# Kernel tuning notes

Measured on AMD Instinct MI355X. Metric: run time of the kernel, lower is better.

The kernel has to match this reference:

```python
import jax, jax.numpy as jnp
import numpy as np

N_NODES = 50000


def setup_inputs() -> dict:
    key = jax.random.key(0)
    k1, k2, k3, k4 = jax.random.split(key, 4)
    x = jax.random.normal(k1, (N_NODES, 128), dtype=jnp.float32)
    edge_index = jax.random.randint(k2, (2, 1600000), 0, N_NODES, dtype=jnp.int64)
    W1 = jax.random.normal(k3, (128, 256), dtype=jnp.float32) * (1.0 / np.sqrt(128))
    b1 = jnp.zeros((256,), dtype=jnp.float32)
    W2 = jax.random.normal(k4, (256, 1), dtype=jnp.float32) * (1.0 / np.sqrt(256))
    b2 = jnp.zeros((1,), dtype=jnp.float32)
    return {"x": x, "edge_index": edge_index, "W1": W1, "b1": b1, "W2": W2, "b2": b2}


def _gcn_conv(x, src, dst, norm, W, b, n_nodes):
    # PyG GCNConv: h = X W; out_i = sum_j norm_ij * h_j (+ self loop) + b
    h = x @ W                               # [N, F_out]
    msg = h[src] * norm[:, None]            # [E', F_out] gather + scale
    out = jax.ops.segment_sum(msg, dst, num_segments=n_nodes)  # scatter-add
    return out + b


def reference(x, edge_index, W1, b1, W2, b2):
    n = x.shape[0]
    loop = jnp.arange(n, dtype=edge_index.dtype)
    src = jnp.concatenate([edge_index[0], loop])   # add self loops
    dst = jnp.concatenate([edge_index[1], loop])
    # symmetric degree normalization on A + I
    deg = jax.ops.segment_sum(jnp.ones_like(dst, dtype=x.dtype), dst, num_segments=n)
    dis = jnp.where(deg > 0, jax.lax.rsqrt(deg), 0.0)
    norm = dis[src] * dis[dst]                     # [E']
    h = jax.nn.relu(_gcn_conv(x, src, dst, norm, W1, b1, n))
    return _gcn_conv(h, src, dst, norm, W2, b2, n)
```

## Files before the change

kernel.cpp:

```cpp
#include <hip/hip_runtime.h>


#define EPB_LOG 12
#define EPB (1 << EPB_LOG)
#define BW_LOG 7
#define BW (1 << BW_LOG)
#define MAXBUCK 512
#define SCAN_TILE 2048
#define AMSTRIDE 136

typedef __attribute__((ext_vector_type(8))) short bf16x8;
typedef __attribute__((ext_vector_type(4))) float f32x4;

__device__ inline unsigned short f2bf(float f) {
    unsigned int b = __float_as_uint(f);
    unsigned int r = b + 0x7FFFu + ((b >> 16) & 1u);
    return (unsigned short)(r >> 16);
}
__device__ inline float bf_lo(unsigned int u) { return __uint_as_float(u << 16); }
__device__ inline float bf_hi(unsigned int u) { return __uint_as_float(u & 0xFFFF0000u); }

__device__ inline void acc8(float* a, uint4 v) {
    a[0] += bf_lo(v.x); a[1] += bf_hi(v.x);
    a[2] += bf_lo(v.y); a[3] += bf_hi(v.y);
    a[4] += bf_lo(v.z); a[5] += bf_hi(v.z);
    a[6] += bf_lo(v.w); a[7] += bf_hi(v.w);
}

__device__ inline int detect_stride(const int* edges, int t, int* sh) {
    if (t < 64) {
        int v = edges[2 * t + 1];
        unsigned long long bb = __ballot(v != 0);
        if (t == 0) *sh = bb ? 1 : 2;
    }
    __syncthreads();
    return *sh;
}


__global__ __launch_bounds__(256) void k_count(
        const int* __restrict__ edges, const float* __restrict__ W1,
        unsigned short* __restrict__ w1t, int* __restrict__ btot_raw,
        long long E, int nbuck, int nsb) {
    int b = blockIdx.x, t = threadIdx.x;
    if (b >= nsb) {
        int row = (b - nsb) * 2 + (t >> 7);
        int k = t & 127;
        w1t[row * 128 + k] = f2bf(W1[k * 256 + row]);
        return;
    }
    __shared__ int bins[MAXBUCK];
    __shared__ int sh;
    for (int i = t; i < nbuck; i += 256) bins[i] = 0;
    int stride = detect_stride(edges, t, &sh);
    long long base = (long long)b << EPB_LOG;
    long long rem = E - base;
    int nE = (rem < (long long)EPB) ? (int)rem : EPB;
    for (int i = t; i < nE; i += 256) {
        int d = edges[(E + base + i) * stride];
        atomicAdd(&bins[d >> BW_LOG], 1);
    }
    __syncthreads();
    for (int i = t; i < nbuck; i += 256)
        if (bins[i]) atomicAdd(&btot_raw[i], bins[i]);
}

__global__ __launch_bounds__(256) void k_btot_scan(
        const int* __restrict__ btot_raw, int* __restrict__ btot,
        int* __restrict__ curg, int nbuck) {
    __shared__ int ws4[4];
    int t = threadIdx.x;
    int c4 = (nbuck + 255) >> 8;
    int lo = t * c4;
    int hi = lo + c4; if (hi > nbuck) hi = nbuck;
    if (lo > nbuck) lo = nbuck;
    int vals[2];
    int local = 0;
    for (int i = lo; i < hi; ++i) { vals[i - lo] = btot_raw[i]; local += vals[i - lo]; }
    int lane = t & 63, w = t >> 6;
    int inc = local;
    for (int off = 1; off < 64; off <<= 1) {
        int u = __shfl_up(inc, off, 64);
        if (lane >= off) inc += u;
    }
    if (lane == 63) ws4[w] = inc;
    __syncthreads();
    int woff = 0;
    for (int i = 0; i < w; ++i) woff += ws4[i];
    int ex = woff + inc - local;
    for (int i = lo; i < hi; ++i) {
        btot[i] = ex; curg[i] = ex;
        ex += vals[i - lo];
    }
}

__global__ __launch_bounds__(256) void k_partition(
        const int* __restrict__ edges, int* __restrict__ curg,
        unsigned int* __restrict__ part, long long E, int nbuck) {
    __shared__ unsigned int stage[EPB];
    __shared__ unsigned short dst16[EPB];
    __shared__ int bins[MAXBUCK];
    __shared__ int lcur[MAXBUCK];
    __shared__ int gbase[MAXBUCK];
    __shared__ int ws4[4];
    __shared__ int sh;
    int sb = blockIdx.x, t = threadIdx.x;
    for (int i = t; i < nbuck; i += 256) bins[i] = 0;
    int stride = detect_stride(edges, t, &sh);
    long long base = (long long)sb << EPB_LOG;
    long long rem = E - base;
    int nE = (rem < (long long)EPB) ? (int)rem : EPB;
    for (int i = t; i < nE; i += 256) {
        int d = edges[(E + base + i) * stride];
        dst16[i] = (unsigned short)d;
        atomicAdd(&bins[d >> BW_LOG], 1);
    }
    __syncthreads();
    int c4 = (nbuck + 255) >> 8;
    int lo = t * c4;
    int hi = lo + c4; if (hi > nbuck) hi = nbuck;
    if (lo > nbuck) lo = nbuck;
    int vals[2];
    int local = 0;
    for (int i = lo; i < hi; ++i) { vals[i - lo] = bins[i]; local += vals[i - lo]; }
    for (int i = t; i < nbuck; i += 256) {
        int c = bins[i];
        gbase[i] = c ? atomicAdd(&curg[i], c) : 0;
    }
    __syncthreads();
    int lane = t & 63, w = t >> 6;
    int inc = local;
    for (int off = 1; off < 64; off <<= 1) {
        int u = __shfl_up(inc, off, 64);
        if (lane >= off) inc += u;
    }
    if (lane == 63) ws4[w] = inc;
    __syncthreads();
    int woff = 0;
    for (int i = 0; i < w; ++i) woff += ws4[i];
    int ex = woff + inc - local;
    for (int i = lo; i < hi; ++i) {
        bins[i] = ex;
        lcur[i] = ex;
        ex += vals[i - lo];
    }
    __syncthreads();
    for (int i = t; i < nE; i += 256) {
        int s = edges[(base + i) * stride];
        int d = dst16[i];
        int b = d >> BW_LOG;
        int p = atomicAdd(&lcur[b], 1);
        stage[p] = ((unsigned int)s << 16) | (unsigned int)d;
    }
    __syncthreads();
    for (int i = t; i < nE; i += 256) {
        unsigned int pk = stage[i];
        int b = (int)(pk & 0xFFFFu) >> BW_LOG;
        part[gbase[b] + (i - bins[b])] = pk;
    }
}

__global__ __launch_bounds__(256) void k_build_csr(
        const unsigned int* __restrict__ part, const int* __restrict__ btot,
        const float* __restrict__ x, int* __restrict__ row_start,
        float* __restrict__ dis, int* __restrict__ csr_src,
        unsigned short* __restrict__ xs, int nbuck, int n, long long E) {
    __shared__ int c128[BW];
    __shared__ int lcur[BW];
    __shared__ float dld[BW];
    __shared__ int ws2[2];
    int b = blockIdx.x, t = threadIdx.x;
    if (t < BW) c128[t] = 0;
    __syncthreads();
    int start = btot[b];
    int endp = (b + 1 < nbuck) ? btot[b + 1] : (int)E;
    for (int i = start + t; i < endp; i += 256)
        atomicAdd(&c128[part[i] & (BW - 1)], 1);
    __syncthreads();
    int lane = t & 63, w = t >> 6;
    int deg = (t < BW) ? c128[t] : 0;
    int inc = deg;
    for (int off = 1; off < 64; off <<= 1) {
        int u = __shfl_up(inc, off, 64);
        if (lane >= off) inc += u;
    }
    if (t < BW && lane == 63) ws2[w] = inc;
    __syncthreads();
    if (t < BW) {
        int ex = inc - deg + ((w == 1) ? ws2[0] : 0);
        lcur[t] = ex;
        int d = (b << BW_LOG) + t;
        if (d < n) {
            row_start[d] = start + ex;
            float dv = rsqrtf((float)deg + 1.0f);
            dis[d] = dv;
            dld[t] = dv;
        }
    }
    if (b == nbuck - 1 && t == 0) row_start[n] = (int)E;
    __syncthreads();
    for (int i = start + t; i < endp; i += 256) {
        unsigned int pk = part[i];
        int r = atomicAdd(&lcur[pk & (BW - 1)], 1);
        csr_src[start + r] = (int)(pk >> 16);
    }
    int d0 = b << BW_LOG;
    for (int idx = t; idx < BW * 32; idx += 256) {
        int node = d0 + (idx >> 5);
        if (node >= n) break;
        float dv = dld[idx >> 5];
        float4 v = ((const float4*)x)[(size_t)node * 32 + (idx & 31)];
        ushort4 o;
        o.x = f2bf(v.x * dv); o.y = f2bf(v.y * dv);
        o.z = f2bf(v.z * dv); o.w = f2bf(v.w * dv);
        ((ushort4*)xs)[(size_t)node * 32 + (idx & 31)] = o;
    }
}

__global__ __launch_bounds__(256) void k_agg_mm(
        const unsigned short* __restrict__ xs, const int* __restrict__ csr_src,
        const int* __restrict__ rs, const float* __restrict__ dis,
        const unsigned short* __restrict__ w1t, const float* __restrict__ b1,
        const float* __restrict__ W2, float* __restrict__ svs, int n) {
    __shared__ short am[16 * AMSTRIDE];
    int t = threadIdx.x;
    int lane = t & 63, w = t >> 6;
    int q = lane >> 4, l16 = lane & 15;
    int blk = blockIdx.x;
    int r = w * 4 + q;
    int node = blk * 16 + r;
    const uint4* xs4 = (const uint4*)xs;

    uint4 o = {0u, 0u, 0u, 0u};
    if (node < n) {
        float a[8] = {0.f, 0.f, 0.f, 0.f, 0.f, 0.f, 0.f, 0.f};
        acc8(a, xs4[((size_t)node << 4) + l16]);
        int start = rs[node], end = rs[node + 1];
        int e = start;
        for (; e + 8 <= end; e += 8) {
            int s0 = csr_src[e],     s1 = csr_src[e + 1];
            int s2 = csr_src[e + 2], s3 = csr_src[e + 3];
            int s4 = csr_src[e + 4], s5 = csr_src[e + 5];
            int s6 = csr_src[e + 6], s7 = csr_src[e + 7];
            uint4 v0 = xs4[((size_t)s0 << 4) + l16];
            uint4 v1 = xs4[((size_t)s1 << 4) + l16];
            uint4 v2 = xs4[((size_t)s2 << 4) + l16];
            uint4 v3 = xs4[((size_t)s3 << 4) + l16];
            uint4 v4 = xs4[((size_t)s4 << 4) + l16];
            uint4 v5 = xs4[((size_t)s5 << 4) + l16];
            uint4 v6 = xs4[((size_t)s6 << 4) + l16];
            uint4 v7 = xs4[((size_t)s7 << 4) + l16];
            acc8(a, v0); acc8(a, v1); acc8(a, v2); acc8(a, v3);
            acc8(a, v4); acc8(a, v5); acc8(a, v6); acc8(a, v7);
        }
        for (; e < end; ++e) {
            int s0 = csr_src[e];
            acc8(a, xs4[((size_t)s0 << 4) + l16]);
        }
        float dn = dis[node];
        o.x = (unsigned int)f2bf(a[0] * dn) | ((unsigned int)f2bf(a[1] * dn) << 16);
        o.y = (unsigned int)f2bf(a[2] * dn) | ((unsigned int)f2bf(a[3] * dn) << 16);
        o.z = (unsigned int)f2bf(a[4] * dn) | ((unsigned int)f2bf(a[5] * dn) << 16);
        o.w = (unsigned int)f2bf(a[6] * dn) | ((unsigned int)f2bf(a[7] * dn) << 16);
    }
    *(uint4*)&am[r * AMSTRIDE + l16 * 8] = o;
    __syncthreads();
    if (w) return;
    int m = lane & 15;
    int quad = lane >> 4;
    int node0 = blk * 16;

    bf16x8 afrag[4];
    const short* arow = &am[m * AMSTRIDE + quad * 8];
#pragma unroll
    for (int ks = 0; ks < 4; ++ks)
        afrag[ks] = *(const bf16x8*)(arow + ks * 32);

    float p0 = 0.f, p1 = 0.f, p2 = 0.f, p3 = 0.f;
#pragma unroll 1
    for (int tt = 0; tt < 16; ++tt) {
        const unsigned short* brow = w1t + (size_t)(tt * 16 + m) * 128 + quad * 8;
        f32x4 acc = {0.f, 0.f, 0.f, 0.f};
#pragma unroll
        for (int ks = 0; ks < 4; ++ks) {
            bf16x8 bfrag = *(const bf16x8*)(brow + ks * 32);
            acc = __builtin_amdgcn_mfma_f32_16x16x32_bf16(afrag[ks], bfrag, acc, 0, 0, 0);
        }
        int col = tt * 16 + m;
        float bb = b1[col], w2 = W2[col];
        float h0 = acc[0] + bb, h1 = acc[1] + bb, h2 = acc[2] + bb, h3 = acc[3] + bb;
        p0 += (h0 > 0.f ? h0 : 0.f) * w2;
        p1 += (h1 > 0.f ? h1 : 0.f) * w2;
        p2 += (h2 > 0.f ? h2 : 0.f) * w2;
        p3 += (h3 > 0.f ? h3 : 0.f) * w2;
    }
#pragma unroll
    for (int off = 1; off < 16; off <<= 1) {
        p0 += __shfl_xor(p0, off, 64);
        p1 += __shfl_xor(p1, off, 64);
        p2 += __shfl_xor(p2, off, 64);
        p3 += __shfl_xor(p3, off, 64);
    }
    if (m == 0) {
        int nb = node0 + quad * 4;
        if (nb + 0 < n) svs[nb + 0] = p0 * dis[nb + 0];
        if (nb + 1 < n) svs[nb + 1] = p1 * dis[nb + 1];
        if (nb + 2 < n) svs[nb + 2] = p2 * dis[nb + 2];
        if (nb + 3 < n) svs[nb + 3] = p3 * dis[nb + 3];
    }
}

__global__ __launch_bounds__(256) void k_out(
        const float* __restrict__ svs, const int* __restrict__ csr_src,
        const int* __restrict__ row_start, const float* __restrict__ dis,
        const float* __restrict__ b2, float* __restrict__ out, int n) {
    int t = threadIdx.x;
    int lane = t & 63, w = t >> 6;
    int q = lane >> 4, l16 = lane & 15;
    int node = blockIdx.x * 16 + w * 4 + q;
    if (node >= n) return;
    int start = row_start[node], end = row_start[node + 1];
    float acc = 0.f;
    for (int e = start + l16; e < end; e += 16)
        acc += svs[csr_src[e]];
#pragma unroll
    for (int off = 1; off < 16; off <<= 1) acc += __shfl_xor(acc, off, 64);
    if (l16 == 0)
        out[node] = dis[node] * (acc + svs[node]) + b2[0];
}

__global__ void k_init(const int* __restrict__ edges, int* __restrict__ flag,
                       int* __restrict__ cnt, int n) {
    int i = blockIdx.x * blockDim.x + threadIdx.x;
    if (i < n) cnt[i] = 0;
    if (blockIdx.x == 0 && threadIdx.x < 64) {
        int v = edges[2 * threadIdx.x + 1];
        unsigned long long b = __ballot(v != 0);
        if (threadIdx.x == 0) flag[0] = b ? 1 : 2;
    }
}
__global__ __launch_bounds__(128) void k_prep_w(const float* __restrict__ W1,
        unsigned short* __restrict__ w1t) {
    int nn = blockIdx.x, k = threadIdx.x;
    w1t[nn * 128 + k] = f2bf(W1[k * 256 + nn]);
}
__global__ __launch_bounds__(256) void k_prep_xs(const float* __restrict__ x,
        const float* __restrict__ dis, unsigned short* __restrict__ xs, int n) {
    int i = blockIdx.x * 256 + threadIdx.x;
    if (i >= n * 32) return;
    float dsc = dis[i >> 5];
    float4 v = ((const float4*)x)[i];
    ushort4 o;
    o.x = f2bf(v.x * dsc); o.y = f2bf(v.y * dsc);
    o.z = f2bf(v.z * dsc); o.w = f2bf(v.w * dsc);
    ((ushort4*)xs)[i] = o;
}
__global__ void k_count_slow(const int* __restrict__ edges, const int* __restrict__ flag,
                             int* __restrict__ cnt, int* __restrict__ posi, long long E) {
    long long e = (long long)blockIdx.x * blockDim.x + threadIdx.x;
    if (e >= E) return;
    int stride = flag[0];
    int d = edges[(E + e) * stride];
    posi[e] = atomicAdd(&cnt[d], 1);
}
__global__ __launch_bounds__(256) void k_scan_partial(
        const int* __restrict__ cnt, int* __restrict__ bsum, int n) {
    int t = threadIdx.x;
    int idx = blockIdx.x * SCAN_TILE + t * 8;
    int s = 0;
#pragma unroll
    for (int j = 0; j < 8; ++j) { int i = idx + j; if (i < n) s += cnt[i]; }
    for (int off = 32; off; off >>= 1) s += __shfl_down(s, off, 64);
    __shared__ int ws[4];
    if ((t & 63) == 0) ws[t >> 6] = s;
    __syncthreads();
    if (t == 0) bsum[blockIdx.x] = ws[0] + ws[1] + ws[2] + ws[3];
}
__global__ void k_scan_tops(int* __restrict__ bsum, int nb) {
    int t = threadIdx.x;
    int w = (t < nb) ? bsum[t] : 0;
    int v = w;
    for (int off = 1; off < 64; off <<= 1) {
        int u = __shfl_up(v, off, 64);
        if (t >= off) v += u;
    }
    if (t < nb) bsum[t] = v - w;
}
__global__ __launch_bounds__(256) void k_scan_apply(
        const int* __restrict__ cnt, const int* __restrict__ bsum,
        int* __restrict__ row_start, float* __restrict__ dis, int n) {
    int t = threadIdx.x;
    int lane = t & 63, w = t >> 6;
    int idx = blockIdx.x * SCAN_TILE + t * 8;
    int vals[8];
    int s = 0;
#pragma unroll
    for (int j = 0; j < 8; ++j) { int i = idx + j; vals[j] = (i < n) ? cnt[i] : 0; s += vals[j]; }
    int inc = s;
    for (int off = 1; off < 64; off <<= 1) {
        int u = __shfl_up(inc, off, 64);
        if (lane >= off) inc += u;
    }
    __shared__ int wsum[4];
    if (lane == 63) wsum[w] = inc;
    __syncthreads();
    int woff = 0;
    for (int i = 0; i < w; ++i) woff += wsum[i];
    int ex = bsum[blockIdx.x] + woff + inc - s;
#pragma unroll
    for (int j = 0; j < 8; ++j) {
        int i = idx + j;
        if (i < n) {
            row_start[i] = ex;
            dis[i] = rsqrtf((float)vals[j] + 1.0f);
            ex += vals[j];
        }
    }
    if (idx <= n && n < idx + 8) row_start[n] = ex;
}
__global__ void k_scatter_slow(const int* __restrict__ edges, const int* __restrict__ flag,
                               const int* __restrict__ row_start, const int* __restrict__ posi,
                               int* __restrict__ csr_src, long long E) {
    long long e = (long long)blockIdx.x * blockDim.x + threadIdx.x;
    if (e >= E) return;
    int stride = flag[0];
    int s = edges[e * stride];
    int d = edges[(E + e) * stride];
    csr_src[row_start[d] + posi[e]] = s;
}
__global__ __launch_bounds__(256) void k_agg(
        const unsigned short* __restrict__ xs, const int* __restrict__ csr_src,
        const int* __restrict__ row_start, const float* __restrict__ dis,
        unsigned short* __restrict__ aggh, int n) {
    int wid  = (blockIdx.x * blockDim.x + threadIdx.x) >> 6;
    int lane = threadIdx.x & 63;
    if (wid >= n) return;
    int start = row_start[wid], end = row_start[wid + 1];
    unsigned int self = ((const unsigned int*)xs)[((size_t)wid << 6) + lane];
    float a0 = bf_lo(self), a1 = bf_hi(self);
    for (int e = start; e < end; ++e) {
        int s0 = csr_src[e];
        unsigned int v0 = ((const unsigned int*)xs)[((size_t)s0 << 6) + lane];
        a0 += bf_lo(v0); a1 += bf_hi(v0);
    }
    float dn = dis[wid];
    unsigned int pack = (unsigned int)f2bf(a0 * dn) | ((unsigned int)f2bf(a1 * dn) << 16);
    ((unsigned int*)aggh)[((size_t)wid << 6) + lane] = pack;
}
__global__ __launch_bounds__(256) void k_mm(
        const unsigned short* __restrict__ aggh, const unsigned short* __restrict__ w1t,
        const float* __restrict__ b1, const float* __restrict__ W2,
        const float* __restrict__ dis, float* __restrict__ svs, int n) {
    int wave = threadIdx.x >> 6;
    int lane = threadIdx.x & 63;
    int m = lane & 15, quad = lane >> 4;
    int node0 = blockIdx.x * 64 + wave * 16;
    bf16x8 afrag[4];
    const unsigned short* arow = aggh + (size_t)(node0 + m) * 128 + quad * 8;
#pragma unroll
    for (int ks = 0; ks < 4; ++ks) afrag[ks] = *(const bf16x8*)(arow + ks * 32);
    float p0 = 0.f, p1 = 0.f, p2 = 0.f, p3 = 0.f;
#pragma unroll 1
    for (int tt = 0; tt < 16; ++tt) {
        const unsigned short* brow = w1t + (size_t)(tt * 16 + m) * 128 + quad * 8;
        f32x4 acc = {0.f, 0.f, 0.f, 0.f};
#pragma unroll
        for (int ks = 0; ks < 4; ++ks) {
            bf16x8 bfrag = *(const bf16x8*)(brow + ks * 32);
            acc = __builtin_amdgcn_mfma_f32_16x16x32_bf16(afrag[ks], bfrag, acc, 0, 0, 0);
        }
        int col = tt * 16 + m;
        float bb = b1[col], w2 = W2[col];
        float h0 = acc[0] + bb, h1 = acc[1] + bb, h2 = acc[2] + bb, h3 = acc[3] + bb;
        p0 += (h0 > 0.f ? h0 : 0.f) * w2;
        p1 += (h1 > 0.f ? h1 : 0.f) * w2;
        p2 += (h2 > 0.f ? h2 : 0.f) * w2;
        p3 += (h3 > 0.f ? h3 : 0.f) * w2;
    }
#pragma unroll
    for (int off = 1; off < 16; off <<= 1) {
        p0 += __shfl_xor(p0, off, 64);
        p1 += __shfl_xor(p1, off, 64);
        p2 += __shfl_xor(p2, off, 64);
        p3 += __shfl_xor(p3, off, 64);
    }
    if (m == 0) {
        int nb = node0 + quad * 4;
        if (nb + 0 < n) svs[nb + 0] = p0 * dis[nb + 0];
        if (nb + 1 < n) svs[nb + 1] = p1 * dis[nb + 1];
        if (nb + 2 < n) svs[nb + 2] = p2 * dis[nb + 2];
        if (nb + 3 < n) svs[nb + 3] = p3 * dis[nb + 3];
    }
}

extern "C" void kernel_launch(void* const* d_in, const int* in_sizes, int n_in,
                              void* d_out, int out_size, void* d_ws, size_t ws_size,
                              hipStream_t stream) {
    const float* x  = (const float*)d_in[0];
    const int*   ei = (const int*)d_in[1];
    const float* W1 = (const float*)d_in[2];
    const float* b1 = (const float*)d_in[3];
    const float* W2 = (const float*)d_in[4];
    const float* b2 = (const float*)d_in[5];
    float* out = (float*)d_out;

    const int N = in_sizes[0] / 128;
    const long long E = in_sizes[1] / 2;
    const int nsb = (int)((E + EPB - 1) >> EPB_LOG);
    const int nbuck = (N + BW - 1) >> BW_LOG;

    char* ws = (char*)d_ws;
    size_t off = 0;
    auto take = [&](size_t bytes) -> char* {
        char* p = ws + off;
        off = (off + bytes + 255) & ~(size_t)255;
        return p;
    };
    int*            flag     = (int*)take(4);
    int*            cnt      = (int*)take((size_t)N * 4);
    int*            rs       = (int*)take((size_t)(N + 1) * 4);
    float*          dis      = (float*)take((size_t)N * 4);
    float*          svs      = (float*)take((size_t)N * 4);
    int*            bsum     = (int*)take(64 * 4);
    int*            btot_raw = (int*)take(MAXBUCK * 4);
    int*            btot     = (int*)take(MAXBUCK * 4);
    int*            curg     = (int*)take(MAXBUCK * 4);
    unsigned int*   part     = (unsigned int*)take((size_t)E * 4);
    int*            csr_src  = (int*)take((size_t)E * 4);
    unsigned short* xs       = (unsigned short*)take((size_t)N * 128 * 2);
    unsigned short* w1t      = (unsigned short*)take((size_t)256 * 128 * 2);
    unsigned short* aggh     = (unsigned short*)take((size_t)(N + 64) * 128 * 2);

    int nb_n  = (N + 255) / 256;
    int nb_e  = (int)((E + 255) / 256);
    int nb_s  = (N + SCAN_TILE - 1) / SCAN_TILE;
    int nb_x  = (N * 32 + 255) / 256;
    int nb_am = (N + 15) / 16;
    int nb_o  = (N + 15) / 16;

    bool fast = (N < 65536);

    if (fast) {
        hipMemsetAsync(btot_raw, 0, (size_t)nbuck * 4, stream);
        k_count    <<<nsb + 128, 256, 0, stream>>>(ei, W1, w1t, btot_raw, E, nbuck, nsb);
        k_btot_scan<<<1, 256, 0, stream>>>(btot_raw, btot, curg, nbuck);
        k_partition<<<nsb, 256, 0, stream>>>(ei, curg, part, E, nbuck);
        k_build_csr<<<nbuck, 256, 0, stream>>>(part, btot, x, rs, dis, csr_src,
                                               xs, nbuck, N, E);
        k_agg_mm   <<<nb_am, 256, 0, stream>>>(xs, csr_src, rs, dis, w1t, b1, W2, svs, N);
        k_out      <<<nb_o, 256, 0, stream>>>(svs, csr_src, rs, dis, b2, out, N);
    } else {
        k_init        <<<nb_n, 256, 0, stream>>>(ei, flag, cnt, N);
        k_prep_w      <<<256, 128, 0, stream>>>(W1, w1t);
        k_count_slow  <<<nb_e, 256, 0, stream>>>(ei, flag, cnt, (int*)part, E);
        k_scan_partial<<<nb_s, 256, 0, stream>>>(cnt, bsum, N);
        k_scan_tops   <<<1, 64, 0, stream>>>(bsum, nb_s);
        k_scan_apply  <<<nb_s, 256, 0, stream>>>(cnt, bsum, rs, dis, N);
        k_prep_xs     <<<nb_x, 256, 0, stream>>>(x, dis, xs, N);
        k_scatter_slow<<<nb_e, 256, 0, stream>>>(ei, flag, rs, (const int*)part, csr_src, E);
        k_agg         <<<(N + 3) / 4, 256, 0, stream>>>(xs, csr_src, rs, dis, aggh, N);
        k_mm          <<<(N + 63) / 64, 256, 0, stream>>>(aggh, w1t, b1, W2, dis, svs, N);
        k_out         <<<nb_o, 256, 0, stream>>>(svs, csr_src, rs, dis, b2, out, N);
    }
}
```

Before: 219.1 us.

## Enlarge agg_mm blocks to 64 nodes and prefetch neighbor indices via shuffles

The fused aggregate+matmul kernel now runs 1024-thread blocks covering 64 nodes, so four wavefronts run the MFMA stage instead of one while the other twelve exit. In the gather loop each 16-lane group loads 16 edge indices cooperatively, prefetches the next 16, and broadcasts them with shuffles, so sixteen row gathers are in flight per step. The aim is to cut serialized index loads and raise memory-level parallelism. In exchange, the larger blocks and the launch-bounds hint of 1024 threads with 8 waves per EU may raise register pressure or limit occupancy.

```diff
diff --git a/kernel.cpp b/kernel.cpp
--- a/kernel.cpp
+++ b/kernel.cpp
@@ -217,18 +217,19 @@
     }
 }
 
-__global__ __launch_bounds__(256) void k_agg_mm(
+__global__ __launch_bounds__(1024, 8) void k_agg_mm(
         const unsigned short* __restrict__ xs, const int* __restrict__ csr_src,
         const int* __restrict__ rs, const float* __restrict__ dis,
         const unsigned short* __restrict__ w1t, const float* __restrict__ b1,
         const float* __restrict__ W2, float* __restrict__ svs, int n) {
-    __shared__ short am[16 * AMSTRIDE];
+    __shared__ short am[64 * AMSTRIDE];
     int t = threadIdx.x;
     int lane = t & 63, w = t >> 6;
     int q = lane >> 4, l16 = lane & 15;
+    int qb = lane & 48;
     int blk = blockIdx.x;
     int r = w * 4 + q;
-    int node = blk * 16 + r;
+    int node = blk * 64 + r;
     const uint4* xs4 = (const uint4*)xs;
 
     uint4 o = {0u, 0u, 0u, 0u};
@@ -237,21 +238,28 @@
         acc8(a, xs4[((size_t)node << 4) + l16]);
         int start = rs[node], end = rs[node + 1];
         int e = start;
-        for (; e + 8 <= end; e += 8) {
-            int s0 = csr_src[e],     s1 = csr_src[e + 1];
-            int s2 = csr_src[e + 2], s3 = csr_src[e + 3];
-            int s4 = csr_src[e + 4], s5 = csr_src[e + 5];
-            int s6 = csr_src[e + 6], s7 = csr_src[e + 7];
-            uint4 v0 = xs4[((size_t)s0 << 4) + l16];
-            uint4 v1 = xs4[((size_t)s1 << 4) + l16];
-            uint4 v2 = xs4[((size_t)s2 << 4) + l16];
-            uint4 v3 = xs4[((size_t)s3 << 4) + l16];
-            uint4 v4 = xs4[((size_t)s4 << 4) + l16];
-            uint4 v5 = xs4[((size_t)s5 << 4) + l16];
-            uint4 v6 = xs4[((size_t)s6 << 4) + l16];
-            uint4 v7 = xs4[((size_t)s7 << 4) + l16];
-            acc8(a, v0); acc8(a, v1); acc8(a, v2); acc8(a, v3);
-            acc8(a, v4); acc8(a, v5); acc8(a, v6); acc8(a, v7);
+        int idx = 0;
+        if (e + 16 <= end) idx = csr_src[e + l16];
+        for (; e + 16 <= end; e += 16) {
+            int pe = e + 16 + l16;
+            int nidx = csr_src[pe < end ? pe : start];
+            int sA[8];
+#pragma unroll
+            for (int j = 0; j < 8; ++j) sA[j] = __shfl(idx, qb + j, 64);
+            uint4 va[8];
+#pragma unroll
+            for (int j = 0; j < 8; ++j) va[j] = xs4[((size_t)sA[j] << 4) + l16];
+#pragma unroll
+            for (int j = 0; j < 8; ++j) acc8(a, va[j]);
+            int sB[8];
+#pragma unroll
+            for (int j = 0; j < 8; ++j) sB[j] = __shfl(idx, qb + 8 + j, 64);
+            uint4 vb[8];
+#pragma unroll
+            for (int j = 0; j < 8; ++j) vb[j] = xs4[((size_t)sB[j] << 4) + l16];
+#pragma unroll
+            for (int j = 0; j < 8; ++j) acc8(a, vb[j]);
+            idx = nidx;
         }
         for (; e < end; ++e) {
             int s0 = csr_src[e];
@@ -265,13 +273,13 @@
     }
     *(uint4*)&am[r * AMSTRIDE + l16 * 8] = o;
     __syncthreads();
-    if (w) return;
+    if (w >= 4) return;
     int m = lane & 15;
     int quad = lane >> 4;
-    int node0 = blk * 16;
+    int node0 = blk * 64 + w * 16;
 
     bf16x8 afrag[4];
-    const short* arow = &am[m * AMSTRIDE + quad * 8];
+    const short* arow = &am[(w * 16 + m) * AMSTRIDE + quad * 8];
 #pragma unroll
     for (int ks = 0; ks < 4; ++ks)
         afrag[ks] = *(const bf16x8*)(arow + ks * 32);
@@ -535,7 +543,7 @@
     int nb_e  = (int)((E + 255) / 256);
     int nb_s  = (N + SCAN_TILE - 1) / SCAN_TILE;
     int nb_x  = (N * 32 + 255) / 256;
-    int nb_am = (N + 15) / 16;
+    int nb_am = (N + 63) / 64;
     int nb_o  = (N + 15) / 16;
 
     bool fast = (N < 65536);
@@ -547,7 +555,7 @@
         k_partition<<<nsb, 256, 0, stream>>>(ei, curg, part, E, nbuck);
         k_build_csr<<<nbuck, 256, 0, stream>>>(part, btot, x, rs, dis, csr_src,
                                                xs, nbuck, N, E);
-        k_agg_mm   <<<nb_am, 256, 0, stream>>>(xs, csr_src, rs, dis, w1t, b1, W2, svs, N);
+        k_agg_mm   <<<nb_am, 1024, 0, stream>>>(xs, csr_src, rs, dis, w1t, b1, W2, svs, N);
         k_out      <<<nb_o, 256, 0, stream>>>(svs, csr_src, rs, dis, b2, out, N);
     } else {
         k_init        <<<nb_n, 256, 0, stream>>>(ei, flag, cnt, N);
```

After: 322.6 us. 47.2% more time.

## Fuse fast-path pipeline into one cooperative persistent kernel with grid syncs

Applied to the files above, without the earlier changes.

Replaces the memset and six separate launches of the fast path with a single cooperative kernel. Each former kernel becomes a phase run by grid-stride loops over a persistent grid sized from the occupancy query, and phases are separated by grid-wide syncs. Phase shared-memory layouts are overlaid in a union. The aim is to remove per-launch overhead and inter-kernel gaps. In exchange, the larger shared footprint and register pressure of one fused kernel may lower occupancy, and grid syncs plus a capped grid may serialize work. The old multi-kernel path is kept as a fallback if the cooperative launch fails.

```diff
diff --git a/kernel.cpp b/kernel.cpp
--- a/kernel.cpp
+++ b/kernel.cpp
@@ -1,4 +1,7 @@
 #include <hip/hip_runtime.h>
+#include <hip/hip_cooperative_groups.h>
+
+namespace cg = cooperative_groups;
 
 
 #define EPB_LOG 12
@@ -35,6 +38,297 @@
     }
     __syncthreads();
     return *sh;
+}
+
+
+struct SPart {
+    unsigned int stage[EPB];
+    unsigned short dst16[EPB];
+    int bins[MAXBUCK];
+    int lcur[MAXBUCK];
+    int gbase[MAXBUCK];
+    int ws4[4];
+    int sh;
+};
+struct SCnt { int bins[MAXBUCK]; int sh; };
+struct SCsr { int c128[BW]; int lcur[BW]; float dld[BW]; int ws2[2]; };
+struct SAgg { short am[16 * AMSTRIDE]; };
+struct SScan { int ws4[4]; };
+union SU { SPart part; SCnt cnt; SCsr csr; SAgg agg; SScan scan; };
+
+__global__ __launch_bounds__(256) void k_all(
+        const int* __restrict__ edges, const float* __restrict__ x,
+        const float* __restrict__ W1, const float* __restrict__ b1,
+        const float* __restrict__ W2, const float* __restrict__ b2,
+        int* __restrict__ btot_raw, int* __restrict__ btot,
+        int* __restrict__ curg, unsigned int* __restrict__ part,
+        int* __restrict__ rs, float* __restrict__ dis,
+        int* __restrict__ csr_src, unsigned short* __restrict__ xs,
+        unsigned short* __restrict__ w1t, float* __restrict__ svs,
+        float* __restrict__ out,
+        long long E, int nbuck, int nsb, int n) {
+    cg::grid_group gg = cg::this_grid();
+    __shared__ SU su;
+    int t = threadIdx.x;
+    int lane = t & 63, w = t >> 6;
+    int q = lane >> 4, l16 = lane & 15;
+    int nblk = gridDim.x;
+
+    for (int i = blockIdx.x * 256 + t; i < nbuck; i += nblk * 256) btot_raw[i] = 0;
+    gg.sync();
+
+    for (int role = blockIdx.x; role < nsb + 128; role += nblk) {
+        if (role >= nsb) {
+            int row = (role - nsb) * 2 + (t >> 7);
+            int k = t & 127;
+            w1t[row * 128 + k] = f2bf(W1[k * 256 + row]);
+        } else {
+            for (int i = t; i < nbuck; i += 256) su.cnt.bins[i] = 0;
+            int stride = detect_stride(edges, t, &su.cnt.sh);
+            long long base = (long long)role << EPB_LOG;
+            long long rem = E - base;
+            int nE = (rem < (long long)EPB) ? (int)rem : EPB;
+            for (int i = t; i < nE; i += 256) {
+                int d = edges[(E + base + i) * stride];
+                atomicAdd(&su.cnt.bins[d >> BW_LOG], 1);
+            }
+            __syncthreads();
+            for (int i = t; i < nbuck; i += 256)
+                if (su.cnt.bins[i]) atomicAdd(&btot_raw[i], su.cnt.bins[i]);
+        }
+        __syncthreads();
+    }
+    gg.sync();
+
+    if (blockIdx.x == 0) {
+        int c4 = (nbuck + 255) >> 8;
+        int lo = t * c4;
+        int hi = lo + c4; if (hi > nbuck) hi = nbuck;
+        if (lo > nbuck) lo = nbuck;
+        int vals[2];
+        int local = 0;
+        for (int i = lo; i < hi; ++i) { vals[i - lo] = btot_raw[i]; local += vals[i - lo]; }
+        int inc = local;
+        for (int off = 1; off < 64; off <<= 1) {
+            int u = __shfl_up(inc, off, 64);
+            if (lane >= off) inc += u;
+        }
+        if (lane == 63) su.scan.ws4[w] = inc;
+        __syncthreads();
+        int woff = 0;
+        for (int i = 0; i < w; ++i) woff += su.scan.ws4[i];
+        int ex = woff + inc - local;
+        for (int i = lo; i < hi; ++i) {
+            btot[i] = ex; curg[i] = ex;
+            ex += vals[i - lo];
+        }
+    }
+    gg.sync();
+
+    for (int sb = blockIdx.x; sb < nsb; sb += nblk) {
+        for (int i = t; i < nbuck; i += 256) su.part.bins[i] = 0;
+        int stride = detect_stride(edges, t, &su.part.sh);
+        long long base = (long long)sb << EPB_LOG;
+        long long rem = E - base;
+        int nE = (rem < (long long)EPB) ? (int)rem : EPB;
+        for (int i = t; i < nE; i += 256) {
+            int d = edges[(E + base + i) * stride];
+            su.part.dst16[i] = (unsigned short)d;
+            atomicAdd(&su.part.bins[d >> BW_LOG], 1);
+        }
+        __syncthreads();
+        int c4 = (nbuck + 255) >> 8;
+        int lo = t * c4;
+        int hi = lo + c4; if (hi > nbuck) hi = nbuck;
+        if (lo > nbuck) lo = nbuck;
+        int vals[2];
+        int local = 0;
+        for (int i = lo; i < hi; ++i) { vals[i - lo] = su.part.bins[i]; local += vals[i - lo]; }
+        for (int i = t; i < nbuck; i += 256) {
+            int c = su.part.bins[i];
+            su.part.gbase[i] = c ? atomicAdd(&curg[i], c) : 0;
+        }
+        __syncthreads();
+        int inc = local;
+        for (int off = 1; off < 64; off <<= 1) {
+            int u = __shfl_up(inc, off, 64);
+            if (lane >= off) inc += u;
+        }
+        if (lane == 63) su.part.ws4[w] = inc;
+        __syncthreads();
+        int woff = 0;
+        for (int i = 0; i < w; ++i) woff += su.part.ws4[i];
+        int ex = woff + inc - local;
+        for (int i = lo; i < hi; ++i) {
+            su.part.bins[i] = ex;
+            su.part.lcur[i] = ex;
+            ex += vals[i - lo];
+        }
+        __syncthreads();
+        for (int i = t; i < nE; i += 256) {
+            int s = edges[(base + i) * stride];
+            int d = su.part.dst16[i];
+            int b = d >> BW_LOG;
+            int p = atomicAdd(&su.part.lcur[b], 1);
+            su.part.stage[p] = ((unsigned int)s << 16) | (unsigned int)d;
+        }
+        __syncthreads();
+        for (int i = t; i < nE; i += 256) {
+            unsigned int pk = su.part.stage[i];
+            int b = (int)(pk & 0xFFFFu) >> BW_LOG;
+            part[su.part.gbase[b] + (i - su.part.bins[b])] = pk;
+        }
+        __syncthreads();
+    }
+    gg.sync();
+
+    for (int b = blockIdx.x; b < nbuck; b += nblk) {
+        if (t < BW) su.csr.c128[t] = 0;
+        __syncthreads();
+        int start = btot[b];
+        int endp = (b + 1 < nbuck) ? btot[b + 1] : (int)E;
+        for (int i = start + t; i < endp; i += 256)
+            atomicAdd(&su.csr.c128[part[i] & (BW - 1)], 1);
+        __syncthreads();
+        int deg = (t < BW) ? su.csr.c128[t] : 0;
+        int inc = deg;
+        for (int off = 1; off < 64; off <<= 1) {
+            int u = __shfl_up(inc, off, 64);
+            if (lane >= off) inc += u;
+        }
+        if (t < BW && lane == 63) su.csr.ws2[w] = inc;
+        __syncthreads();
+        if (t < BW) {
+            int ex = inc - deg + ((w == 1) ? su.csr.ws2[0] : 0);
+            su.csr.lcur[t] = ex;
+            int d = (b << BW_LOG) + t;
+            if (d < n) {
+                rs[d] = start + ex;
+                float dv = rsqrtf((float)deg + 1.0f);
+                dis[d] = dv;
+                su.csr.dld[t] = dv;
+            }
+        }
+        if (b == nbuck - 1 && t == 0) rs[n] = (int)E;
+        __syncthreads();
+        for (int i = start + t; i < endp; i += 256) {
+            unsigned int pk = part[i];
+            int r2 = atomicAdd(&su.csr.lcur[pk & (BW - 1)], 1);
+            csr_src[start + r2] = (int)(pk >> 16);
+        }
+        int d0 = b << BW_LOG;
+        for (int idx = t; idx < BW * 32; idx += 256) {
+            int node = d0 + (idx >> 5);
+            if (node >= n) break;
+            float dv = su.csr.dld[idx >> 5];
+            float4 v = ((const float4*)x)[(size_t)node * 32 + (idx & 31)];
+            ushort4 o;
+            o.x = f2bf(v.x * dv); o.y = f2bf(v.y * dv);
+            o.z = f2bf(v.z * dv); o.w = f2bf(v.w * dv);
+            ((ushort4*)xs)[(size_t)node * 32 + (idx & 31)] = o;
+        }
+        __syncthreads();
+    }
+    gg.sync();
+
+    int ntile = (n + 15) >> 4;
+    const uint4* xs4 = (const uint4*)xs;
+    for (int blk = blockIdx.x; blk < ntile; blk += nblk) {
+        int r = w * 4 + q;
+        int node = blk * 16 + r;
+        uint4 o = {0u, 0u, 0u, 0u};
+        if (node < n) {
+            float a[8] = {0.f, 0.f, 0.f, 0.f, 0.f, 0.f, 0.f, 0.f};
+            acc8(a, xs4[((size_t)node << 4) + l16]);
+            int start = rs[node], end = rs[node + 1];
+            int e = start;
+            for (; e + 8 <= end; e += 8) {
+                int s0 = csr_src[e],     s1 = csr_src[e + 1];
+                int s2 = csr_src[e + 2], s3 = csr_src[e + 3];
+                int s4 = csr_src[e + 4], s5 = csr_src[e + 5];
+                int s6 = csr_src[e + 6], s7 = csr_src[e + 7];
+                uint4 v0 = xs4[((size_t)s0 << 4) + l16];
+                uint4 v1 = xs4[((size_t)s1 << 4) + l16];
+                uint4 v2 = xs4[((size_t)s2 << 4) + l16];
+                uint4 v3 = xs4[((size_t)s3 << 4) + l16];
+                uint4 v4 = xs4[((size_t)s4 << 4) + l16];
+                uint4 v5 = xs4[((size_t)s5 << 4) + l16];
+                uint4 v6 = xs4[((size_t)s6 << 4) + l16];
+                uint4 v7 = xs4[((size_t)s7 << 4) + l16];
+                acc8(a, v0); acc8(a, v1); acc8(a, v2); acc8(a, v3);
+                acc8(a, v4); acc8(a, v5); acc8(a, v6); acc8(a, v7);
+            }
+            for (; e < end; ++e) {
+                int s0 = csr_src[e];
+                acc8(a, xs4[((size_t)s0 << 4) + l16]);
+            }
+            float dn = dis[node];
+            o.x = (unsigned int)f2bf(a[0] * dn) | ((unsigned int)f2bf(a[1] * dn) << 16);
+            o.y = (unsigned int)f2bf(a[2] * dn) | ((unsigned int)f2bf(a[3] * dn) << 16);
+            o.z = (unsigned int)f2bf(a[4] * dn) | ((unsigned int)f2bf(a[5] * dn) << 16);
+            o.w = (unsigned int)f2bf(a[6] * dn) | ((unsigned int)f2bf(a[7] * dn) << 16);
+        }
+        *(uint4*)&su.agg.am[r * AMSTRIDE + l16 * 8] = o;
+        __syncthreads();
+        if (w == 0) {
+            int m = lane & 15;
+            int quad = lane >> 4;
+            int node0 = blk * 16;
+            bf16x8 afrag[4];
+            const short* arow = &su.agg.am[m * AMSTRIDE + quad * 8];
+#pragma unroll
+            for (int ks = 0; ks < 4; ++ks)
+                afrag[ks] = *(const bf16x8*)(arow + ks * 32);
+            float p0 = 0.f, p1 = 0.f, p2 = 0.f, p3 = 0.f;
+#pragma unroll 1
+            for (int tt = 0; tt < 16; ++tt) {
+                const unsigned short* brow = w1t + (size_t)(tt * 16 + m) * 128 + quad * 8;
+                f32x4 acc = {0.f, 0.f, 0.f, 0.f};
+#pragma unroll
+                for (int ks = 0; ks < 4; ++ks) {
+                    bf16x8 bfrag = *(const bf16x8*)(brow + ks * 32);
+                    acc = __builtin_amdgcn_mfma_f32_16x16x32_bf16(afrag[ks], bfrag, acc, 0, 0, 0);
+                }
+                int col = tt * 16 + m;
+                float bb = b1[col], w2v = W2[col];
+                float h0 = acc[0] + bb, h1 = acc[1] + bb, h2 = acc[2] + bb, h3 = acc[3] + bb;
+                p0 += (h0 > 0.f ? h0 : 0.f) * w2v;
+                p1 += (h1 > 0.f ? h1 : 0.f) * w2v;
+                p2 += (h2 > 0.f ? h2 : 0.f) * w2v;
+                p3 += (h3 > 0.f ? h3 : 0.f) * w2v;
+            }
+#pragma unroll
+            for (int off = 1; off < 16; off <<= 1) {
+                p0 += __shfl_xor(p0, off, 64);
+                p1 += __shfl_xor(p1, off, 64);
+                p2 += __shfl_xor(p2, off, 64);
+                p3 += __shfl_xor(p3, off, 64);
+            }
+            if (m == 0) {
+                int nb = node0 + quad * 4;
+                if (nb + 0 < n) svs[nb + 0] = p0 * dis[nb + 0];
+                if (nb + 1 < n) svs[nb + 1] = p1 * dis[nb + 1];
+                if (nb + 2 < n) svs[nb + 2] = p2 * dis[nb + 2];
+                if (nb + 3 < n) svs[nb + 3] = p3 * dis[nb + 3];
+            }
+        }
+        __syncthreads();
+    }
+    gg.sync();
+
+    for (int ob = blockIdx.x; ob < ntile; ob += nblk) {
+        int node = ob * 16 + w * 4 + q;
+        if (node < n) {
+            int start = rs[node], end = rs[node + 1];
+            float acc = 0.f;
+            for (int e = start + l16; e < end; e += 16)
+                acc += svs[csr_src[e]];
+#pragma unroll
+            for (int off = 1; off < 16; off <<= 1) acc += __shfl_xor(acc, off, 64);
+            if (l16 == 0)
+                out[node] = dis[node] * (acc + svs[node]) + b2[0];
+        }
+    }
 }
 
 
@@ -230,7 +524,6 @@
     int r = w * 4 + q;
     int node = blk * 16 + r;
     const uint4* xs4 = (const uint4*)xs;
-
     uint4 o = {0u, 0u, 0u, 0u};
     if (node < n) {
         float a[8] = {0.f, 0.f, 0.f, 0.f, 0.f, 0.f, 0.f, 0.f};
@@ -269,13 +562,11 @@
     int m = lane & 15;
     int quad = lane >> 4;
     int node0 = blk * 16;
-
     bf16x8 afrag[4];
     const short* arow = &am[m * AMSTRIDE + quad * 8];
 #pragma unroll
     for (int ks = 0; ks < 4; ++ks)
         afrag[ks] = *(const bf16x8*)(arow + ks * 32);
-
     float p0 = 0.f, p1 = 0.f, p2 = 0.f, p3 = 0.f;
 #pragma unroll 1
     for (int tt = 0; tt < 16; ++tt) {
@@ -505,9 +796,9 @@
     float* out = (float*)d_out;
 
     const int N = in_sizes[0] / 128;
-    const long long E = in_sizes[1] / 2;
-    const int nsb = (int)((E + EPB - 1) >> EPB_LOG);
-    const int nbuck = (N + BW - 1) >> BW_LOG;
+    long long E = in_sizes[1] / 2;
+    int nsb = (int)((E + EPB - 1) >> EPB_LOG);
+    int nbuck = (N + BW - 1) >> BW_LOG;
 
     char* ws = (char*)d_ws;
     size_t off = 0;
@@ -541,14 +832,34 @@
     bool fast = (N < 65536);
 
     if (fast) {
-        hipMemsetAsync(btot_raw, 0, (size_t)nbuck * 4, stream);
-        k_count    <<<nsb + 128, 256, 0, stream>>>(ei, W1, w1t, btot_raw, E, nbuck, nsb);
-        k_btot_scan<<<1, 256, 0, stream>>>(btot_raw, btot, curg, nbuck);
-        k_partition<<<nsb, 256, 0, stream>>>(ei, curg, part, E, nbuck);
-        k_build_csr<<<nbuck, 256, 0, stream>>>(part, btot, x, rs, dis, csr_src,
-                                               xs, nbuck, N, E);
-        k_agg_mm   <<<nb_am, 256, 0, stream>>>(xs, csr_src, rs, dis, w1t, b1, W2, svs, N);
-        k_out      <<<nb_o, 256, 0, stream>>>(svs, csr_src, rs, dis, b2, out, N);
+        int Nv = N;
+        int occb = 0;
+        hipError_t qerr = hipOccupancyMaxActiveBlocksPerMultiprocessor(&occb, k_all, 256, 0);
+        int grid = 768;
+        if (qerr == hipSuccess && occb > 0) {
+            long long g = (long long)occb * 256;
+            if (g > 1024) g = 1024;
+            if (g < 256) g = 256;
+            grid = (int)g;
+        }
+        void* kargs[] = {
+            (void*)&ei, (void*)&x, (void*)&W1, (void*)&b1, (void*)&W2, (void*)&b2,
+            (void*)&btot_raw, (void*)&btot, (void*)&curg, (void*)&part,
+            (void*)&rs, (void*)&dis, (void*)&csr_src, (void*)&xs, (void*)&w1t,
+            (void*)&svs, (void*)&out, (void*)&E, (void*)&nbuck, (void*)&nsb, (void*)&Nv
+        };
+        hipError_t cerr = hipLaunchCooperativeKernel((void*)k_all, dim3(grid), dim3(256),
+                                                     kargs, 0, stream);
+        if (cerr != hipSuccess) {
+            hipMemsetAsync(btot_raw, 0, (size_t)nbuck * 4, stream);
+            k_count    <<<nsb + 128, 256, 0, stream>>>(ei, W1, w1t, btot_raw, E, nbuck, nsb);
+            k_btot_scan<<<1, 256, 0, stream>>>(btot_raw, btot, curg, nbuck);
+            k_partition<<<nsb, 256, 0, stream>>>(ei, curg, part, E, nbuck);
+            k_build_csr<<<nbuck, 256, 0, stream>>>(part, btot, x, rs, dis, csr_src,
+                                                   xs, nbuck, N, E);
+            k_agg_mm   <<<nb_am, 256, 0, stream>>>(xs, csr_src, rs, dis, w1t, b1, W2, svs, N);
+            k_out      <<<nb_o, 256, 0, stream>>>(svs, csr_src, rs, dis, b2, out, N);
+        }
     } else {
         k_init        <<<nb_n, 256, 0, stream>>>(ei, flag, cnt, N);
         k_prep_w      <<<256, 128, 0, stream>>>(W1, w1t);
```

Result: slower. 577.6 us (+163.6%).
